# Kernel optimization log

Measured on AMD Instinct MI355X. Metric: run time of the kernel, lower is better.

Reference implementation:

```python
import math
import jax, jax.numpy as jnp
import numpy as np


def setup_inputs() -> dict:
    key = jax.random.key(0)
    k1, k2, k3 = jax.random.split(key, 3)
    B, T, D = 4, 2048, 2048
    x = jax.random.normal(k1, (B, T, D), dtype=jnp.float32)
    w_qkv = jax.random.normal(k2, (D, 3 * D), dtype=jnp.float32) * 0.02
    w_proj = jax.random.normal(k3, (D, D), dtype=jnp.float32) * 0.02
    b_proj = jnp.zeros((D,), dtype=jnp.float32)
    return {"x": x, "w_qkv": w_qkv, "w_proj": w_proj, "b_proj": b_proj, "n_head": 16}


def reference(x, w_qkv, w_proj, b_proj, n_head):
    B, T, D = x.shape
    N = n_head
    H = D // N
    qkv = x @ w_qkv                       # (B,T,3D)
    q, k, v = jnp.split(qkv, 3, axis=-1)  # each (B,T,D)
    # NOTE: original torch code does .view(B, n_head, T, H) directly on the
    # (B,T,D) tensor (a raw memory reinterpretation, not a head split+transpose).
    q = q.reshape(B, N, T, H)
    k = k.reshape(B, N, T, H)
    v = v.reshape(B, N, T, H)
    # full T x T score matrix, scaled by sqrt(D) (not sqrt(H)) as in the original
    a = jnp.einsum('bnih,bnjh->bnij', q, k) / math.sqrt(D)  # (B,N,T,T)
    a = jax.nn.softmax(a, axis=3)
    # torch.einsum('bntt,bnth->bnth', a, v): repeated 't' in first operand
    # takes the DIAGONAL of the attention matrix, then elementwise-scales v.
    diag = jnp.diagonal(a, axis1=2, axis2=3)  # (B,N,T)
    o = diag[..., None] * v                   # (B,N,T,H)
    o = jnp.transpose(o, (0, 2, 1, 3)).reshape(B, T, D)
    return o @ w_proj + b_proj
```

## Files before the change

kernel.cpp:

```cpp
#include <hip/hip_runtime.h>
#include <hip/hip_bf16.h>

typedef short bf16x8 __attribute__((ext_vector_type(8)));
typedef float f32x4 __attribute__((ext_vector_type(4)));

__device__ __forceinline__ unsigned short f2bf(float f) {
  union { float f; unsigned int u; } x; x.f = f;
  return (unsigned short)((x.u + 0x7fffu + ((x.u >> 16) & 1u)) >> 16);
}
__device__ __forceinline__ float bf2f(unsigned short u) {
  union { unsigned int u; float f; } x; x.u = ((unsigned int)u) << 16;
  return x.f;
}
__device__ __forceinline__ void gload_lds16(const void* g, void* l) {
  __builtin_amdgcn_global_load_lds((const __attribute__((address_space(1))) void*)g,
                                   (__attribute__((address_space(3))) void*)l, 16, 0, 0);
}

__global__ void cast_f32_bf16(const float* __restrict__ src, unsigned short* __restrict__ dst) {
  int i = blockIdx.x * blockDim.x + threadIdx.x;
  float4 v = reinterpret_cast<const float4*>(src)[i];
  ushort4 o;
  o.x = f2bf(v.x); o.y = f2bf(v.y); o.z = f2bf(v.z); o.w = f2bf(v.w);
  reinterpret_cast<ushort4*>(dst)[i] = o;
}

__global__ void transpose_cast(const float* __restrict__ src, unsigned short* __restrict__ dst,
                               int R, int C) {
  __shared__ float tile[32][33];
  int c0 = blockIdx.x * 32, r0 = blockIdx.y * 32;
  int tx = threadIdx.x, ty = threadIdx.y;
#pragma unroll
  for (int i = 0; i < 4; ++i)
    tile[ty + i * 8][tx] = src[(size_t)(r0 + ty + i * 8) * C + (c0 + tx)];
  __syncthreads();
#pragma unroll
  for (int i = 0; i < 4; ++i)
    dst[(size_t)(c0 + ty + i * 8) * R + (r0 + tx)] = f2bf(tile[tx][ty + i * 8]);
}

template <int EPI>
__global__ __launch_bounds__(512, 2)
void gemm256(const unsigned short* __restrict__ A, const unsigned short* __restrict__ Bt,
             unsigned short* __restrict__ Qo, unsigned short* __restrict__ Ko,
             unsigned short* __restrict__ Vo, float* __restrict__ Cf,
             const float* __restrict__ bias, int M, int N, int K) {
  extern __shared__ __align__(16) char lds[];
  const int tid = threadIdx.x;
  const int lane = tid & 63, wid = tid >> 6;
  const int wm = wid >> 2, wn = wid & 3;
  const int fr = lane & 15, fq = lane >> 4;

  const int nbn = N >> 8;
  const int cpx = gridDim.x >> 3;
  const int id = blockIdx.x;
  const int sw = (id & 7) * cpx + (id >> 3);
  const int bm = sw / nbn, bn = sw % nbn;
  const int row0 = bm << 8, col0 = bn << 8;

  const int NT = K >> 6;

  const int srow = tid >> 3;
  const int scol = ((tid & 7) ^ (srow & 7)) << 3;

  const unsigned short* qA0 = A + (size_t)(row0 + srow) * K + scol;
  const unsigned short* qA1 = A + (size_t)(row0 + 128 + srow) * K + scol;
  const unsigned short* qB0 = Bt + (size_t)(col0 + srow) * K + scol;
  const unsigned short* qB1 = Bt + (size_t)(col0 + 128 + srow) * K + scol;
  const unsigned short* dummy = A + (tid << 3);
  const size_t K64 = (size_t)64 * K;

  auto stageTo = [&](const unsigned short* src, int slot) {
    char* l0 = lds + slot * 16384 + tid * 16;
    gload_lds16(src, l0);
    gload_lds16(src + K64, l0 + 8192);
  };

  auto rdA = [&](const char* base, bf16x8 (&dst)[4][2]) {
#pragma unroll
    for (int i2 = 0; i2 < 4; ++i2)
#pragma unroll
      for (int ks = 0; ks < 2; ++ks) {
        const int byte = ((((wm * 4 + i2) * 16 + fr) * 128) + ks * 64 + fq * 16) ^ ((fr & 7) << 4);
        dst[i2][ks] = *reinterpret_cast<const bf16x8*>(base + byte);
      }
  };
  auto rdB = [&](const char* base, bf16x8 (&dst)[2][2]) {
#pragma unroll
    for (int j2 = 0; j2 < 2; ++j2)
#pragma unroll
      for (int ks = 0; ks < 2; ++ks) {
        const int byte = ((((wn * 2 + j2) * 16 + fr) * 128) + ks * 64 + fq * 16) ^ ((fr & 7) << 4);
        dst[j2][ks] = *reinterpret_cast<const bf16x8*>(base + byte);
      }
  };

  f32x4 acc[2][4][2][2] = {};

  stageTo(qA0, 0); stageTo(qB0, 1); stageTo(qB1, 2); stageTo(qA1, 3);
  stageTo(qA0 + 64, 4); stageTo(qB0 + 64, 5);
  asm volatile("s_waitcnt vmcnt(6)" ::: "memory");
  asm volatile("s_barrier" ::: "memory");

  auto body = [&](int sb, int s0, int s1, int s2, int s3,
                  const unsigned short* pB1, const unsigned short* pA1,
                  const unsigned short* pA0, const unsigned short* pB0,
                  bool g01, bool g23) {
    const char* As0 = lds + (sb + 0) * 16384;
    const char* Bs0 = lds + (sb + 1) * 16384;
    const char* Bs1 = lds + (sb + 2) * 16384;
    const char* As1 = lds + (sb + 3) * 16384;
    bf16x8 a[4][2], b0[2][2], b1[2][2];

    rdA(As0, a);
    rdB(Bs0, b0);
    stageTo(g01 ? pB1 : dummy, s0);
    asm volatile("s_waitcnt vmcnt(6)" ::: "memory");
    __builtin_amdgcn_s_setprio(1);
#pragma unroll
    for (int i2 = 0; i2 < 4; ++i2)
#pragma unroll
      for (int j2 = 0; j2 < 2; ++j2)
#pragma unroll
        for (int ks = 0; ks < 2; ++ks)
          acc[0][i2][0][j2] =
              __builtin_amdgcn_mfma_f32_16x16x32_bf16(a[i2][ks], b0[j2][ks], acc[0][i2][0][j2], 0, 0, 0);
    __builtin_amdgcn_s_setprio(0);

    rdB(Bs1, b1);
    stageTo(g01 ? pA1 : dummy, s1);
    asm volatile("s_waitcnt vmcnt(6)" ::: "memory");
    asm volatile("s_barrier" ::: "memory");
    __builtin_amdgcn_s_setprio(1);
#pragma unroll
    for (int i2 = 0; i2 < 4; ++i2)
#pragma unroll
      for (int j2 = 0; j2 < 2; ++j2)
#pragma unroll
        for (int ks = 0; ks < 2; ++ks)
          acc[0][i2][1][j2] =
              __builtin_amdgcn_mfma_f32_16x16x32_bf16(a[i2][ks], b1[j2][ks], acc[0][i2][1][j2], 0, 0, 0);
    __builtin_amdgcn_s_setprio(0);

    rdA(As1, a);
    stageTo(g23 ? pA0 : dummy, s2);
    asm volatile("s_waitcnt vmcnt(6)" ::: "memory");
    __builtin_amdgcn_s_setprio(1);
#pragma unroll
    for (int i2 = 0; i2 < 4; ++i2)
#pragma unroll
      for (int j2 = 0; j2 < 2; ++j2)
#pragma unroll
        for (int ks = 0; ks < 2; ++ks)
          acc[1][i2][0][j2] =
              __builtin_amdgcn_mfma_f32_16x16x32_bf16(a[i2][ks], b0[j2][ks], acc[1][i2][0][j2], 0, 0, 0);
    __builtin_amdgcn_s_setprio(0);

    stageTo(g23 ? pB0 : dummy, s3);
    asm volatile("s_waitcnt vmcnt(6)" ::: "memory");
    asm volatile("s_barrier" ::: "memory");
    __builtin_amdgcn_s_setprio(1);
#pragma unroll
    for (int i2 = 0; i2 < 4; ++i2)
#pragma unroll
      for (int j2 = 0; j2 < 2; ++j2)
#pragma unroll
        for (int ks = 0; ks < 2; ++ks)
          acc[1][i2][1][j2] =
              __builtin_amdgcn_mfma_f32_16x16x32_bf16(a[i2][ks], b1[j2][ks], acc[1][i2][1][j2], 0, 0, 0);
    __builtin_amdgcn_s_setprio(0);
  };

  const unsigned short* rB1 = qB1 + 64;
  const unsigned short* rA1 = qA1 + 64;
  const unsigned short* rA0 = qA0 + 128;
  const unsigned short* rB0 = qB0 + 128;

  for (int k = 0; k < NT; k += 2) {
    body(0, 6, 7, 0, 1, rB1, rA1, rA0, rB0, k < NT - 1, k < NT - 2);
    body(4, 2, 3, 4, 5, rB1 + 64, rA1 + 64, rA0 + 64, rB0 + 64, k < NT - 2, k < NT - 3);
    rB1 += 128; rA1 += 128; rA0 += 128; rB0 += 128;
  }

  asm volatile("s_waitcnt vmcnt(0)" ::: "memory");

#pragma unroll
  for (int mh = 0; mh < 2; ++mh)
#pragma unroll
    for (int i2 = 0; i2 < 4; ++i2) {
      const int rbase = row0 + (mh * 8 + wm * 4 + i2) * 16 + fq * 4;
#pragma unroll
      for (int nh = 0; nh < 2; ++nh)
#pragma unroll
        for (int j2 = 0; j2 < 2; ++j2) {
          const int col = col0 + (nh * 8 + wn * 2 + j2) * 16 + fr;
#pragma unroll
          for (int r = 0; r < 4; ++r) {
            const float v = acc[mh][i2][nh][j2][r];
            const int row = rbase + r;
            if (EPI == 0) {
              const int seg = col >> 11, cc = col & 2047;
              unsigned short* dst = (seg == 0) ? Qo : (seg == 1 ? Ko : Vo);
              dst[(size_t)row * 2048 + cc] = f2bf(v);
            } else {
              Cf[(size_t)row * N + col] = v + bias[col];
            }
          }
        }
    }
}

__global__ __launch_bounds__(512, 2)
void attn_diag_ov(const unsigned short* __restrict__ Q, const unsigned short* __restrict__ K,
                  const unsigned short* __restrict__ V, unsigned short* __restrict__ OV) {
  __shared__ __align__(16) char ks[3][128 * 256];
  __shared__ float dlds[512];
  const int tid = threadIdx.x;
  const int lane = tid & 63, wid = tid >> 6;
  const int d = blockIdx.x;
  const int head = d & 63, tb = d >> 6;
  const int b = head >> 4, n = head & 15;
  const int t0 = tb << 9;
  const size_t hoff = (size_t)head << 18;
  const unsigned short* Qh = Q + hoff;
  const unsigned short* Kh = K + hoff;
  const unsigned short* Vh = V + hoff;

  const int fr = lane & 15, fq = lane >> 4;
  const int g4 = fq << 2;
  const int qrow0 = t0 + wid * 64;

  bf16x8 qf[4][4];
#pragma unroll
  for (int m = 0; m < 4; ++m)
#pragma unroll
    for (int kk = 0; kk < 4; ++kk)
      qf[m][kk] = *reinterpret_cast<const bf16x8*>(
          Qh + (size_t)(qrow0 + m * 16 + fr) * 128 + kk * 32 + fq * 8);

  auto stageK = [&](int tile, int s) {
    const char* ksrc = (const char*)(Kh + ((size_t)(tile << 7) << 7));
#pragma unroll
    for (int i = 0; i < 4; ++i) {
      const int flat = i * 8192 + tid * 16;
      const int row = flat >> 8, c = (flat >> 4) & 15;
      const int sb = (row << 8) + ((c ^ (row & 15)) << 4);
      gload_lds16(ksrc + sb, &ks[s][0] + flat);
    }
  };

  float rsum[4][4] = {};
  float dnum[4][4] = {};
  const float scale = 0.02209708691207961f;

  stageK(0, 0);
  stageK(1, 1);
  asm volatile("s_waitcnt vmcnt(4)" ::: "memory");
  asm volatile("s_barrier" ::: "memory");

  for (int t = 0; t < 16; ++t) {
    if (t < 14) {
      int s = t + 2; s -= (s >= 3) ? 3 : 0; s -= (s >= 3) ? 3 : 0;
      stageK(t + 2, (t + 2) % 3);
    }
    int cb = t % 3;
    const char* buf = &ks[cb][0];
    const int jc = t << 7;
#pragma unroll
    for (int jt = 0; jt < 8; ++jt) {
      bf16x8 bfrag[4];
#pragma unroll
      for (int kk = 0; kk < 4; ++kk) {
        const int row = jt * 16 + fr;
        const int s = kk * 4 + fq;
        bfrag[kk] = *reinterpret_cast<const bf16x8*>(buf + (row << 8) + ((s ^ (row & 15)) << 4));
      }
      const int colj = jc + jt * 16 + fr;
#pragma unroll
      for (int m = 0; m < 4; ++m) {
        f32x4 acc = {0.f, 0.f, 0.f, 0.f};
#pragma unroll
        for (int kk = 0; kk < 4; ++kk)
          acc = __builtin_amdgcn_mfma_f32_16x16x32_bf16(qf[m][kk], bfrag[kk], acc, 0, 0, 0);
        const int rowt = qrow0 + m * 16 + g4;
#pragma unroll
        for (int r = 0; r < 4; ++r) {
          const float e = __expf(acc[r] * scale);
          rsum[m][r] += e;
          if (colj == rowt + r) dnum[m][r] = e;
        }
      }
    }
    asm volatile("s_waitcnt vmcnt(4)" ::: "memory");
    asm volatile("s_barrier" ::: "memory");
  }

#pragma unroll
  for (int m = 0; m < 4; ++m)
#pragma unroll
    for (int r = 0; r < 4; ++r) {
#pragma unroll
      for (int s = 1; s < 16; s <<= 1) {
        rsum[m][r] += __shfl_xor(rsum[m][r], s, 64);
        dnum[m][r] += __shfl_xor(dnum[m][r], s, 64);
      }
      if (fr == 0) dlds[wid * 64 + m * 16 + g4 + r] = dnum[m][r] / rsum[m][r];
    }
  __syncthreads();

  const unsigned short* vsrc = Vh + ((size_t)t0 << 7);
  unsigned short* dst = OV + ((size_t)((b << 11) + t0)) * 2048 + (n << 7);
#pragma unroll
  for (int c = 0; c < 16; ++c) {
    const int flat = (c * 512 + tid) << 3;
    const int row = flat >> 7, col = flat & 127;
    bf16x8 v = *reinterpret_cast<const bf16x8*>(vsrc + flat);
    const float dd = dlds[row];
    bf16x8 o;
#pragma unroll
    for (int e = 0; e < 8; ++e)
      o[e] = (short)f2bf(bf2f((unsigned short)v[e]) * dd);
    *reinterpret_cast<bf16x8*>(dst + (size_t)row * 2048 + col) = o;
  }
}

extern "C" void kernel_launch(void* const* d_in, const int* in_sizes, int n_in,
                              void* d_out, int out_size, void* d_ws, size_t ws_size,
                              hipStream_t stream) {
  const float* x = (const float*)d_in[0];
  const float* w_qkv = (const float*)d_in[1];
  const float* w_proj = (const float*)d_in[2];
  const float* b_proj = (const float*)d_in[3];
  float* out = (float*)d_out;

  char* p = (char*)d_ws;
  unsigned short* Xb = (unsigned short*)p;     p += (size_t)8192 * 2048 * 2;
  unsigned short* WqkvT = (unsigned short*)p;  p += (size_t)6144 * 2048 * 2;
  unsigned short* WprojT = (unsigned short*)p; p += (size_t)2048 * 2048 * 2;
  unsigned short* Qb = (unsigned short*)p;     p += (size_t)8192 * 2048 * 2;
  unsigned short* Kb = (unsigned short*)p;     p += (size_t)8192 * 2048 * 2;
  unsigned short* Vb = (unsigned short*)p;     p += (size_t)8192 * 2048 * 2;
  unsigned short* OV = (unsigned short*)p;     p += (size_t)8192 * 2048 * 2;

  (void)hipFuncSetAttribute((const void*)gemm256<0>,
                            hipFuncAttributeMaxDynamicSharedMemorySize, 131072);
  (void)hipFuncSetAttribute((const void*)gemm256<1>,
                            hipFuncAttributeMaxDynamicSharedMemorySize, 131072);

  cast_f32_bf16<<<16384, 256, 0, stream>>>(x, Xb);
  transpose_cast<<<dim3(192, 64), dim3(32, 8), 0, stream>>>(w_qkv, WqkvT, 2048, 6144);
  transpose_cast<<<dim3(64, 64), dim3(32, 8), 0, stream>>>(w_proj, WprojT, 2048, 2048);

  gemm256<0><<<dim3(32 * 24), 512, 131072, stream>>>(Xb, WqkvT, Qb, Kb, Vb, nullptr, nullptr,
                                                     8192, 6144, 2048);
  attn_diag_ov<<<dim3(256), 512, 0, stream>>>(Qb, Kb, Vb, OV);
  gemm256<1><<<dim3(32 * 8), 512, 131072, stream>>>(OV, WprojT, nullptr, nullptr, nullptr, out,
                                                    b_proj, 8192, 2048, 2048);
}
```

Baseline: 339.2 us.

## Prefetch GEMM LDS fragments one phase ahead with separate register sets

The GEMM main loop now keeps separate A0/A1/B0/B1 fragment registers and reads the next phase's operands from LDS (including the next iteration's A0/B0 buffers) before the MFMA block that precedes their use. This is meant to hide LDS read latency behind matrix instructions. Because the extra live fragments raise register pressure, launch bounds drop from two blocks per CU to one, trading occupancy for the deeper software pipeline. The attention loop also gets a small cleanup that removes an unused index computation.

```diff
diff --git a/kernel.cpp b/kernel.cpp
--- a/kernel.cpp
+++ b/kernel.cpp
@@ -40,7 +40,7 @@
 }
 
 template <int EPI>
-__global__ __launch_bounds__(512, 2)
+__global__ __launch_bounds__(512, 1)
 void gemm256(const unsigned short* __restrict__ A, const unsigned short* __restrict__ Bt,
              unsigned short* __restrict__ Qo, unsigned short* __restrict__ Ko,
              unsigned short* __restrict__ Vo, float* __restrict__ Cf,
@@ -96,24 +96,25 @@
   };
 
   f32x4 acc[2][4][2][2] = {};
+  bf16x8 A0[4][2], A1[4][2], B0[2][2], B1[2][2];
 
   stageTo(qA0, 0); stageTo(qB0, 1); stageTo(qB1, 2); stageTo(qA1, 3);
   stageTo(qA0 + 64, 4); stageTo(qB0 + 64, 5);
   asm volatile("s_waitcnt vmcnt(6)" ::: "memory");
   asm volatile("s_barrier" ::: "memory");
+  rdA(lds + 0 * 16384, A0);
+  rdB(lds + 1 * 16384, B0);
 
   auto body = [&](int sb, int s0, int s1, int s2, int s3,
                   const unsigned short* pB1, const unsigned short* pA1,
                   const unsigned short* pA0, const unsigned short* pB0,
                   bool g01, bool g23) {
-    const char* As0 = lds + (sb + 0) * 16384;
-    const char* Bs0 = lds + (sb + 1) * 16384;
     const char* Bs1 = lds + (sb + 2) * 16384;
     const char* As1 = lds + (sb + 3) * 16384;
-    bf16x8 a[4][2], b0[2][2], b1[2][2];
-
-    rdA(As0, a);
-    rdB(Bs0, b0);
+    const char* nAs0 = lds + ((sb ^ 4) + 0) * 16384;
+    const char* nBs0 = lds + ((sb ^ 4) + 1) * 16384;
+
+    rdB(Bs1, B1);
     stageTo(g01 ? pB1 : dummy, s0);
     asm volatile("s_waitcnt vmcnt(6)" ::: "memory");
     __builtin_amdgcn_s_setprio(1);
@@ -124,13 +125,13 @@
 #pragma unroll
         for (int ks = 0; ks < 2; ++ks)
           acc[0][i2][0][j2] =
-              __builtin_amdgcn_mfma_f32_16x16x32_bf16(a[i2][ks], b0[j2][ks], acc[0][i2][0][j2], 0, 0, 0);
+              __builtin_amdgcn_mfma_f32_16x16x32_bf16(A0[i2][ks], B0[j2][ks], acc[0][i2][0][j2], 0, 0, 0);
     __builtin_amdgcn_s_setprio(0);
 
-    rdB(Bs1, b1);
     stageTo(g01 ? pA1 : dummy, s1);
     asm volatile("s_waitcnt vmcnt(6)" ::: "memory");
     asm volatile("s_barrier" ::: "memory");
+    rdA(As1, A1);
     __builtin_amdgcn_s_setprio(1);
 #pragma unroll
     for (int i2 = 0; i2 < 4; ++i2)
@@ -139,10 +140,10 @@
 #pragma unroll
         for (int ks = 0; ks < 2; ++ks)
           acc[0][i2][1][j2] =
-              __builtin_amdgcn_mfma_f32_16x16x32_bf16(a[i2][ks], b1[j2][ks], acc[0][i2][1][j2], 0, 0, 0);
+              __builtin_amdgcn_mfma_f32_16x16x32_bf16(A0[i2][ks], B1[j2][ks], acc[0][i2][1][j2], 0, 0, 0);
     __builtin_amdgcn_s_setprio(0);
 
-    rdA(As1, a);
+    rdA(nAs0, A0);
     stageTo(g23 ? pA0 : dummy, s2);
     asm volatile("s_waitcnt vmcnt(6)" ::: "memory");
     __builtin_amdgcn_s_setprio(1);
@@ -153,12 +154,13 @@
 #pragma unroll
         for (int ks = 0; ks < 2; ++ks)
           acc[1][i2][0][j2] =
-              __builtin_amdgcn_mfma_f32_16x16x32_bf16(a[i2][ks], b0[j2][ks], acc[1][i2][0][j2], 0, 0, 0);
+              __builtin_amdgcn_mfma_f32_16x16x32_bf16(A1[i2][ks], B0[j2][ks], acc[1][i2][0][j2], 0, 0, 0);
     __builtin_amdgcn_s_setprio(0);
 
     stageTo(g23 ? pB0 : dummy, s3);
     asm volatile("s_waitcnt vmcnt(6)" ::: "memory");
     asm volatile("s_barrier" ::: "memory");
+    rdB(nBs0, B0);
     __builtin_amdgcn_s_setprio(1);
 #pragma unroll
     for (int i2 = 0; i2 < 4; ++i2)
@@ -167,7 +169,7 @@
 #pragma unroll
         for (int ks = 0; ks < 2; ++ks)
           acc[1][i2][1][j2] =
-              __builtin_amdgcn_mfma_f32_16x16x32_bf16(a[i2][ks], b1[j2][ks], acc[1][i2][1][j2], 0, 0, 0);
+              __builtin_amdgcn_mfma_f32_16x16x32_bf16(A1[i2][ks], B1[j2][ks], acc[1][i2][1][j2], 0, 0, 0);
     __builtin_amdgcn_s_setprio(0);
   };
 
@@ -259,12 +261,8 @@
   asm volatile("s_barrier" ::: "memory");
 
   for (int t = 0; t < 16; ++t) {
-    if (t < 14) {
-      int s = t + 2; s -= (s >= 3) ? 3 : 0; s -= (s >= 3) ? 3 : 0;
-      stageK(t + 2, (t + 2) % 3);
-    }
-    int cb = t % 3;
-    const char* buf = &ks[cb][0];
+    if (t < 14) stageK(t + 2, (t + 2) % 3);
+    const char* buf = &ks[t % 3][0];
     const int jc = t << 7;
 #pragma unroll
     for (int jt = 0; jt < 8; ++jt) {
```

Result: slower. 679.8 us (+100.4%).
